# Kernel tuning notes

Measured on AMD Instinct MI355X. Metric: run time of the kernel, lower is better.

## Reference

```python
import jax, jax.numpy as jnp
import numpy as np

B, T, SLATE, D = 256, 16, 20, 256
N_ITEMS, N_USERS = 100000, 10000


def setup_inputs() -> dict:
    key = jax.random.key(0)
    ks = jax.random.split(key, 8)
    s = 1.0 / np.sqrt(D)  # PyTorch GRU/Linear init scale ~ U(-1/sqrt(H), 1/sqrt(H))
    return {
        "item_idxs": jax.random.randint(ks[0], (B, T, SLATE), 0, N_ITEMS),
        "user_idxs": jax.random.randint(ks[1], (B, T), 0, N_USERS),
        "responses": jnp.zeros((B, T, SLATE), jnp.float32),
        "item_table": jax.random.normal(ks[2], (N_ITEMS, D), jnp.float32) * 0.02,
        "user_table": jax.random.normal(ks[3], (N_USERS, D), jnp.float32) * 0.02,
        "W_ih": jax.random.uniform(ks[4], (3 * D, 2 * D), jnp.float32, -s, s),
        "W_hh": jax.random.uniform(ks[5], (3 * D, D), jnp.float32, -s, s),
        "b_ih": jnp.zeros((3 * D,), jnp.float32),
        "b_hh": jnp.zeros((3 * D,), jnp.float32),
        "W_out": jax.random.uniform(ks[6], (1, D), jnp.float32, -s, s),
        "b_out": jnp.zeros((1,), jnp.float32),
    }


def _gru_cell(x, h, W_ih, W_hh, b_ih, b_hh):
    # PyTorch GRUCell math. x: [N, 2D], h: [N, D]
    gi = x @ W_ih.T + b_ih  # [N, 3D]
    gh = h @ W_hh.T + b_hh  # [N, 3D]
    i_r, i_z, i_n = jnp.split(gi, 3, axis=-1)
    h_r, h_z, h_n = jnp.split(gh, 3, axis=-1)
    r = jax.nn.sigmoid(i_r + h_r)
    z = jax.nn.sigmoid(i_z + h_z)
    n = jnp.tanh(i_n + r * h_n)
    return (1.0 - z) * n + z * h


def reference(item_idxs, user_idxs, responses, item_table, user_table,
              W_ih, W_hh, b_ih, b_hh, W_out, b_out):
    # embedding lookup: item_embs [B,T,S,D], user_embs [B,T,D]
    item_embs = item_table[item_idxs]
    user_embs = user_table[user_idxs]
    N = B * T
    e = item_embs.reshape(N, SLATE, D).transpose(1, 0, 2)  # [S, N, D]
    h0 = user_embs.reshape(N, D)
    m0 = jnp.ones((N, 1), item_embs.dtype)  # 'soft' readout multiplier, 1 at step 0

    def step(carry, e_i):
        h, m = carry
        x = jnp.concatenate([e_i, e_i * m], axis=-1)  # [N, 2D]
        h = _gru_cell(x, h, W_ih, W_hh, b_ih, b_hh)
        y = h @ W_out.T + b_out  # [N, 1]
        return (h, jax.nn.sigmoid(y)), y[:, 0]

    _, ys = jax.lax.scan(step, (h0, m0), e)  # ys: [S, N]
    return ys.transpose(1, 0).reshape(B, T, SLATE)
```

## Files before the change

### kernel.cpp

```cpp
#include <hip/hip_runtime.h>
#include <math.h>

#define SLATE 20
#define DD 256
#define NSEQ 4096

typedef __attribute__((ext_vector_type(8))) short bf16x8;
typedef __attribute__((ext_vector_type(4))) float f32x4;
typedef unsigned short u16;
typedef unsigned int u32;

__device__ __forceinline__ u16 f2bf(float f) {
    unsigned u = __float_as_uint(f);
    u += 0x7fff + ((u >> 16) & 1);
    return (u16)(u >> 16);
}
__device__ __forceinline__ float blo(u32 u) { return __uint_as_float(u << 16); }
__device__ __forceinline__ float bhi(u32 u) { return __uint_as_float(u & 0xffff0000u); }
__device__ __forceinline__ float sigm_(float x) {
    return __builtin_amdgcn_rcpf(1.f + __builtin_amdgcn_exp2f(-1.44269504f * x));
}
__device__ __forceinline__ float tanh_(float x) {
    return 1.f - 2.f * __builtin_amdgcn_rcpf(1.f + __builtin_amdgcn_exp2f(2.88539008f * x));
}

__device__ __forceinline__ void gl_lds16(const void* g, void* l) {
    __builtin_amdgcn_global_load_lds(
        (const __attribute__((address_space(1))) unsigned int*)g,
        (__attribute__((address_space(3))) unsigned int*)l, 16, 0, 0);
}

__global__ void prep_w(const float* __restrict__ W_ih, const float* __restrict__ W_hh,
                       u16* __restrict__ W12, u16* __restrict__ Whh) {
    int i = blockIdx.x * 256 + threadIdx.x;
    if (i < 1536 * 256) {
        int j = i >> 8, k = i & 255;
        float v = (j < 768) ? W_ih[(size_t)j * 512 + k]
                            : W_ih[(size_t)(j - 768) * 512 + 256 + k];
        W12[i] = f2bf(v);
    } else {
        int i2 = i - 1536 * 256;
        Whh[i2] = f2bf(W_hh[i2]);
    }
}

__global__ void gather_e(int s0, const int* __restrict__ idxs, const float* __restrict__ itab,
                         u16* __restrict__ e_bf) {
    int g = blockIdx.x * 256 + threadIdx.x;
    int row = g >> 6, c = g & 63;
    int n = row & (NSEQ - 1), s = s0 + (row >> 12);
    int idx = idxs[n * SLATE + s];
    float4 v = *(const float4*)&itab[(size_t)idx * DD + c * 4];
    ushort4 o;
    o.x = f2bf(v.x); o.y = f2bf(v.y); o.z = f2bf(v.z); o.w = f2bf(v.w);
    *(ushort4*)&e_bf[(size_t)row * DD + c * 4] = o;
}

__global__ __launch_bounds__(256) void gemm_e(
        const u16* __restrict__ e_bf, const u16* __restrict__ W12,
        const float* __restrict__ b_ih, const float* __restrict__ b_hh,
        u16* __restrict__ Ge) {
    __shared__ u16 A_s[128][32];
    __shared__ u16 B_s[128][32];

    const int tid = threadIdx.x;
    const int w = tid >> 6, l = tid & 63, lm = l & 15, lq = l >> 4;
    const int wm = w & 1, wn = w >> 1;
    const size_t m0 = (size_t)blockIdx.y * 128;
    const size_t n0 = (size_t)blockIdx.x * 128;

    f32x4 acc[4][4];
    f32x4 zero4 = {0.f, 0.f, 0.f, 0.f};
#pragma unroll
    for (int mi = 0; mi < 4; ++mi)
#pragma unroll
        for (int nj = 0; nj < 4; ++nj) acc[mi][nj] = zero4;

    const int srow = w * 16 + (l >> 2);
    const int skc = (l & 3) * 8;
    const u16* gA = e_bf + (m0 + srow) * DD + skc;
    const u16* gB = W12 + (n0 + srow) * DD + skc;
    u16* lA = &A_s[0][0] + w * 512 + l * 8;
    u16* lB = &B_s[0][0] + w * 512 + l * 8;

    for (int kt = 0; kt < 8; ++kt) {
        const int ko = kt * 32;
        gl_lds16(gA + ko, lA);
        gl_lds16(gA + 64 * DD + ko, lA + 2048);
        gl_lds16(gB + ko, lB);
        gl_lds16(gB + 64 * DD + ko, lB + 2048);
        __syncthreads();
        bf16x8 af[4], bfr[4];
#pragma unroll
        for (int mi = 0; mi < 4; ++mi)
            af[mi] = *(const bf16x8*)&A_s[wm * 64 + mi * 16 + lm][lq * 8];
#pragma unroll
        for (int nj = 0; nj < 4; ++nj)
            bfr[nj] = *(const bf16x8*)&B_s[wn * 64 + nj * 16 + lm][lq * 8];
#pragma unroll
        for (int nj = 0; nj < 4; ++nj)
#pragma unroll
            for (int mi = 0; mi < 4; ++mi)
                acc[mi][nj] = __builtin_amdgcn_mfma_f32_16x16x32_bf16(af[mi], bfr[nj], acc[mi][nj], 0, 0, 0);
        __syncthreads();
    }
    float bb[4];
#pragma unroll
    for (int nj = 0; nj < 4; ++nj) {
        int col = (int)n0 + wn * 64 + nj * 16 + lm;
        bb[nj] = 0.f;
        if (col < 768) bb[nj] = b_ih[col] + (col < 512 ? b_hh[col] : 0.f);
    }
#pragma unroll
    for (int mi = 0; mi < 4; ++mi)
#pragma unroll
        for (int rr = 0; rr < 4; ++rr) {
            u16* gp = Ge + (m0 + wm * 64 + mi * 16 + lq * 4 + rr) * 1536 + n0 + wn * 64 + lm;
#pragma unroll
            for (int nj = 0; nj < 4; ++nj) gp[nj * 16] = f2bf(acc[mi][nj][rr] + bb[nj]);
        }
}

__device__ __forceinline__ int hA_off(int seq, int kt, int lq2) {
    int v = ((kt & 3) << 2) | lq2;
    return kt * 512 + lq2 * 128 + ((seq ^ v) << 3);
}

__global__ __launch_bounds__(512, 2) void seq_kernel(
        int s0, int C,
        const u16* __restrict__ Ge,
        const u16* __restrict__ Whh,
        const int* __restrict__ user_idxs, const float* __restrict__ user_table,
        const float* __restrict__ b_hh,
        const float* __restrict__ W_out, const float* __restrict__ b_out,
        float* __restrict__ h_g, float* __restrict__ m_g, float* __restrict__ out)
{
    __shared__ u16   hA[4096];
    __shared__ float gh_s[16][770];
    __shared__ u16   geL[2][16][1536];

    const int tid = threadIdx.x;
    const int w = tid >> 6, l = tid & 63, lm = l & 15, lq = l >> 4;
    const int l5 = l & 31, sh = l >> 5;
    const int n0 = blockIdx.x * 16;
    const int sloc = 2 * w + sh;
    const int nw = n0 + sloc;
    const int jw2 = w * 96;

    bf16x8 warr[6][8];
    const u16* wb = Whh + (size_t)(jw2 + lm) * DD + lq * 8;
#pragma unroll
    for (int fi = 0; fi < 6; ++fi)
#pragma unroll
        for (int kt = 0; kt < 8; ++kt)
            warr[fi][kt] = *(const bf16x8*)(wb + fi * 16 * DD + kt * 32);

    float bn[6];
#pragma unroll
    for (int fi = 0; fi < 6; ++fi) {
        int colb = jw2 + fi * 16;
        bn[fi] = (colb >= 512) ? b_hh[colb + lm] : 0.f;
    }

    float wo[8];
#pragma unroll
    for (int j = 0; j < 4; ++j) {
        float2 t = *(const float2*)&W_out[2 * l5 + 64 * j];
        wo[2 * j] = t.x; wo[2 * j + 1] = t.y;
    }
    const float bo = b_out[0];

    float h_reg[8]; float m_w;
    if (s0 == 0) {
        const float* hu = user_table + (size_t)user_idxs[nw] * DD;
#pragma unroll
        for (int j = 0; j < 4; ++j) {
            float2 t = *(const float2*)&hu[2 * l5 + 64 * j];
            h_reg[2 * j] = t.x; h_reg[2 * j + 1] = t.y;
        }
        m_w = 1.f;
    } else {
        const float* hp = h_g + (size_t)nw * DD;
#pragma unroll
        for (int j = 0; j < 4; ++j) {
            float2 t = *(const float2*)&hp[2 * l5 + 64 * j];
            h_reg[2 * j] = t.x; h_reg[2 * j + 1] = t.y;
        }
        m_w = m_g[nw];
    }
#pragma unroll
    for (int j = 0; j < 4; ++j) {
        int ktw = (l5 >> 4) + 2 * j, lq2 = (l5 & 15) >> 2;
        u32 pk = (u32)f2bf(h_reg[2 * j]) | ((u32)f2bf(h_reg[2 * j + 1]) << 16);
        *(u32*)&hA[hA_off(sloc, ktw, lq2) + 2 * (l5 & 3)] = pk;
    }

    {
        const u16* g0 = Ge + (size_t)n0 * 1536;
        u16* l0 = &geL[0][0][0];
#pragma unroll
        for (int i = 0; i < 6; ++i)
            gl_lds16(g0 + tid * 8 + i * 4096, l0 + tid * 8 + i * 4096);
    }
    asm volatile("s_waitcnt lgkmcnt(0)" ::: "memory");
    __builtin_amdgcn_s_barrier();
    __builtin_amdgcn_sched_barrier(0);

    for (int sc = 0; sc < C; ++sc) {
        const int cur = sc & 1;

        if (sc + 1 < C) {
            const u16* gn = Ge + ((size_t)(sc + 1) * NSEQ + n0) * 1536;
            u16* ln = &geL[cur ^ 1][0][0];
#pragma unroll
            for (int i = 0; i < 6; ++i)
                gl_lds16(gn + tid * 8 + i * 4096, ln + tid * 8 + i * 4096);
        }
        __builtin_amdgcn_sched_barrier(0);

        f32x4 zero4 = {0.f, 0.f, 0.f, 0.f};
        f32x4 acc[6];
#pragma unroll
        for (int fi = 0; fi < 6; ++fi) acc[fi] = zero4;
#pragma unroll
        for (int kt = 0; kt < 8; ++kt) {
            bf16x8 af = *(const bf16x8*)&hA[hA_off(lm, kt, lq)];
#pragma unroll
            for (int fi = 0; fi < 6; ++fi)
                acc[fi] = __builtin_amdgcn_mfma_f32_16x16x32_bf16(af, warr[fi][kt], acc[fi], 0, 0, 0);
        }
#pragma unroll
        for (int fi = 0; fi < 6; ++fi)
#pragma unroll
            for (int rr = 0; rr < 4; ++rr)
                gh_s[lq * 4 + rr][jw2 + fi * 16 + lm] = acc[fi][rr] + bn[fi];

        if (sc + 1 < C) { asm volatile("s_waitcnt vmcnt(6) lgkmcnt(0)" ::: "memory"); }
        else            { asm volatile("s_waitcnt vmcnt(0) lgkmcnt(0)" ::: "memory"); }
        __builtin_amdgcn_s_barrier();
        __builtin_amdgcn_sched_barrier(0);

        const u32* grow = (const u32*)&geL[cur][sloc][0];
        float yv = 0.f;
#pragma unroll
        for (int j = 0; j < 4; ++j) {
            u32 g1r = grow[      l5 + 32 * j];
            u32 g1z = grow[128 + l5 + 32 * j];
            u32 g1n = grow[256 + l5 + 32 * j];
            u32 g2r = grow[384 + l5 + 32 * j];
            u32 g2z = grow[512 + l5 + 32 * j];
            u32 g2n = grow[640 + l5 + 32 * j];
            const int d0 = 2 * l5 + 64 * j;
            float2 ghr = *(const float2*)&gh_s[sloc][d0];
            float2 ghz = *(const float2*)&gh_s[sloc][256 + d0];
            float2 ghn = *(const float2*)&gh_s[sloc][512 + d0];
            float ir_lo = fmaf(m_w, blo(g2r), blo(g1r));
            float ir_hi = fmaf(m_w, bhi(g2r), bhi(g1r));
            float iz_lo = fmaf(m_w, blo(g2z), blo(g1z));
            float iz_hi = fmaf(m_w, bhi(g2z), bhi(g1z));
            float in_lo = fmaf(m_w, blo(g2n), blo(g1n));
            float in_hi = fmaf(m_w, bhi(g2n), bhi(g1n));
            float r_lo = sigm_(ir_lo + ghr.x);
            float r_hi = sigm_(ir_hi + ghr.y);
            float z_lo = sigm_(iz_lo + ghz.x);
            float z_hi = sigm_(iz_hi + ghz.y);
            float n_lo = tanh_(fmaf(r_lo, ghn.x, in_lo));
            float n_hi = tanh_(fmaf(r_hi, ghn.y, in_hi));
            float hn_lo = fmaf(z_lo, h_reg[2 * j] - n_lo, n_lo);
            float hn_hi = fmaf(z_hi, h_reg[2 * j + 1] - n_hi, n_hi);
            h_reg[2 * j] = hn_lo; h_reg[2 * j + 1] = hn_hi;
            int ktw = (l5 >> 4) + 2 * j, lq2 = (l5 & 15) >> 2;
            u32 pk = (u32)f2bf(hn_lo) | ((u32)f2bf(hn_hi) << 16);
            *(u32*)&hA[hA_off(sloc, ktw, lq2) + 2 * (l5 & 3)] = pk;
            yv += hn_lo * wo[2 * j] + hn_hi * wo[2 * j + 1];
        }
#pragma unroll
        for (int off = 16; off > 0; off >>= 1) yv += __shfl_xor(yv, off, 32);
        float y = yv + bo;
        if (l5 == 0) out[(size_t)nw * SLATE + (s0 + sc)] = y;
        m_w = sigm_(y);

        asm volatile("s_waitcnt lgkmcnt(0)" ::: "memory");
        __builtin_amdgcn_s_barrier();
        __builtin_amdgcn_sched_barrier(0);
    }

#pragma unroll
    for (int j = 0; j < 4; ++j) {
        float2 v; v.x = h_reg[2 * j]; v.y = h_reg[2 * j + 1];
        *(float2*)&h_g[(size_t)nw * DD + 2 * l5 + 64 * j] = v;
    }
    if (l5 == 0) m_g[nw] = m_w;
}

extern "C" void kernel_launch(void* const* d_in, const int* in_sizes, int n_in,
                              void* d_out, int out_size, void* d_ws, size_t ws_size,
                              hipStream_t stream) {
    const int*   item_idxs  = (const int*)d_in[0];
    const int*   user_idxs  = (const int*)d_in[1];
    const float* item_table = (const float*)d_in[3];
    const float* user_table = (const float*)d_in[4];
    const float* W_ih       = (const float*)d_in[5];
    const float* W_hh       = (const float*)d_in[6];
    const float* b_ih       = (const float*)d_in[7];
    const float* b_hh       = (const float*)d_in[8];
    const float* W_out      = (const float*)d_in[9];
    const float* b_out      = (const float*)d_in[10];
    float* out = (float*)d_out;

    const size_t fixed = 786432ull + 393216ull + 4194304ull + 16384ull;
    static const int cands[5] = {10, 5, 4, 2, 1};
    int C = 1;
    for (int i = 0; i < 5; ++i) {
        size_t need = (size_t)cands[i] * (12582912ull + 2097152ull) + fixed;
        if (need <= ws_size) { C = cands[i]; break; }
    }

    u16*   Ge   = (u16*)d_ws;
    u16*   e_bf = (u16*)((char*)d_ws + (size_t)C * 12582912ull);
    u16*   W12  = (u16*)((char*)e_bf + (size_t)C * 2097152ull);
    u16*   Whh  = (u16*)((char*)W12 + 786432ull);
    float* h_g  = (float*)((char*)Whh + 393216ull);
    float* m_g  = (float*)((char*)h_g + 4194304ull);

    prep_w<<<2304, 256, 0, stream>>>(W_ih, W_hh, W12, Whh);

    for (int s0 = 0; s0 < SLATE; s0 += C) {
        gather_e<<<C * 1024, 256, 0, stream>>>(s0, item_idxs, item_table, e_bf);
        dim3 gg(12, 32 * C);
        gemm_e<<<gg, 256, 0, stream>>>(e_bf, W12, b_ih, b_hh, Ge);
        seq_kernel<<<256, 512, 0, stream>>>(s0, C, Ge, Whh, user_idxs, user_table,
                                            b_hh, W_out, b_out, h_g, m_g, out);
    }
}
```

Baseline: 399.2 us.

## Triple-buffer gemm_e LDS loads and vectorize transposed epilogue stores

The input-projection GEMM moves from a single-buffered LDS tile with two barriers per k-step to a three-stage ring. Loads run two k-steps ahead and are tracked with explicit vmcnt waits and one barrier per step. The MFMA operands are swapped so each lane holds four consecutive output columns, which lets the epilogue write packed 8-byte stores instead of scalar 2-byte stores, with the bias loaded before the loop. The cost is triple the LDS footprint and hand-written waitcnt logic that must match the async load count.

```diff
diff --git a/kernel.cpp b/kernel.cpp
--- a/kernel.cpp
+++ b/kernel.cpp
@@ -60,8 +60,8 @@
         const u16* __restrict__ e_bf, const u16* __restrict__ W12,
         const float* __restrict__ b_ih, const float* __restrict__ b_hh,
         u16* __restrict__ Ge) {
-    __shared__ u16 A_s[128][32];
-    __shared__ u16 B_s[128][32];
+    __shared__ u16 A_s[3][128][32];
+    __shared__ u16 B_s[3][128][32];
 
     const int tid = threadIdx.x;
     const int w = tid >> 6, l = tid & 63, lm = l & 15, lq = l >> 4;
@@ -69,6 +69,17 @@
     const size_t m0 = (size_t)blockIdx.y * 128;
     const size_t n0 = (size_t)blockIdx.x * 128;
 
+    float bb[4][4];
+#pragma unroll
+    for (int nj = 0; nj < 4; ++nj)
+#pragma unroll
+        for (int rr = 0; rr < 4; ++rr) {
+            int col = (int)n0 + wn * 64 + nj * 16 + lq * 4 + rr;
+            bb[nj][rr] = 0.f;
+            if (col < 768) bb[nj][rr] = b_ih[col] + (col < 512 ? b_hh[col] : 0.f);
+        }
+    __builtin_amdgcn_sched_barrier(0);
+
     f32x4 acc[4][4];
     f32x4 zero4 = {0.f, 0.f, 0.f, 0.f};
 #pragma unroll
@@ -80,45 +91,58 @@
     const int skc = (l & 3) * 8;
     const u16* gA = e_bf + (m0 + srow) * DD + skc;
     const u16* gB = W12 + (n0 + srow) * DD + skc;
-    u16* lA = &A_s[0][0] + w * 512 + l * 8;
-    u16* lB = &B_s[0][0] + w * 512 + l * 8;
-
+    const int loff = w * 512 + l * 8;
+
+#define STAGE_KT(bi, kk) do { const int ko_ = (kk) * 32;                     \
+        gl_lds16(gA + ko_,            &A_s[bi][0][0] + loff);                \
+        gl_lds16(gA + 64 * DD + ko_,  &A_s[bi][0][0] + loff + 2048);         \
+        gl_lds16(gB + ko_,            &B_s[bi][0][0] + loff);                \
+        gl_lds16(gB + 64 * DD + ko_,  &B_s[bi][0][0] + loff + 2048); } while (0)
+
+    STAGE_KT(0, 0);
+    STAGE_KT(1, 1);
+    asm volatile("s_waitcnt vmcnt(4)" ::: "memory");
+    __builtin_amdgcn_s_barrier();
+    __builtin_amdgcn_sched_barrier(0);
+
+#pragma unroll
     for (int kt = 0; kt < 8; ++kt) {
-        const int ko = kt * 32;
-        gl_lds16(gA + ko, lA);
-        gl_lds16(gA + 64 * DD + ko, lA + 2048);
-        gl_lds16(gB + ko, lB);
-        gl_lds16(gB + 64 * DD + ko, lB + 2048);
-        __syncthreads();
+        const int cur = kt % 3;
+        if (kt + 2 < 8) STAGE_KT((kt + 2) % 3, kt + 2);
+        __builtin_amdgcn_sched_barrier(0);
+
         bf16x8 af[4], bfr[4];
 #pragma unroll
         for (int mi = 0; mi < 4; ++mi)
-            af[mi] = *(const bf16x8*)&A_s[wm * 64 + mi * 16 + lm][lq * 8];
+            af[mi] = *(const bf16x8*)&A_s[cur][wm * 64 + mi * 16 + lm][lq * 8];
 #pragma unroll
         for (int nj = 0; nj < 4; ++nj)
-            bfr[nj] = *(const bf16x8*)&B_s[wn * 64 + nj * 16 + lm][lq * 8];
+            bfr[nj] = *(const bf16x8*)&B_s[cur][wn * 64 + nj * 16 + lm][lq * 8];
 #pragma unroll
         for (int nj = 0; nj < 4; ++nj)
 #pragma unroll
             for (int mi = 0; mi < 4; ++mi)
-                acc[mi][nj] = __builtin_amdgcn_mfma_f32_16x16x32_bf16(af[mi], bfr[nj], acc[mi][nj], 0, 0, 0);
-        __syncthreads();
-    }
-    float bb[4];
-#pragma unroll
-    for (int nj = 0; nj < 4; ++nj) {
-        int col = (int)n0 + wn * 64 + nj * 16 + lm;
-        bb[nj] = 0.f;
-        if (col < 768) bb[nj] = b_ih[col] + (col < 512 ? b_hh[col] : 0.f);
-    }
-#pragma unroll
-    for (int mi = 0; mi < 4; ++mi)
-#pragma unroll
-        for (int rr = 0; rr < 4; ++rr) {
-            u16* gp = Ge + (m0 + wm * 64 + mi * 16 + lq * 4 + rr) * 1536 + n0 + wn * 64 + lm;
-#pragma unroll
-            for (int nj = 0; nj < 4; ++nj) gp[nj * 16] = f2bf(acc[mi][nj][rr] + bb[nj]);
-        }
+                acc[mi][nj] = __builtin_amdgcn_mfma_f32_16x16x32_bf16(bfr[nj], af[mi], acc[mi][nj], 0, 0, 0);
+
+        if (kt < 6) { asm volatile("s_waitcnt vmcnt(4) lgkmcnt(0)" ::: "memory"); }
+        else        { asm volatile("s_waitcnt vmcnt(0) lgkmcnt(0)" ::: "memory"); }
+        __builtin_amdgcn_s_barrier();
+        __builtin_amdgcn_sched_barrier(0);
+    }
+#undef STAGE_KT
+
+#pragma unroll
+    for (int mi = 0; mi < 4; ++mi) {
+        const size_t row = m0 + wm * 64 + mi * 16 + lm;
+#pragma unroll
+        for (int nj = 0; nj < 4; ++nj) {
+            f32x4 a = acc[mi][nj];
+            u32 p0 = (u32)f2bf(a[0] + bb[nj][0]) | ((u32)f2bf(a[1] + bb[nj][1]) << 16);
+            u32 p1 = (u32)f2bf(a[2] + bb[nj][2]) | ((u32)f2bf(a[3] + bb[nj][3]) << 16);
+            uint2 v; v.x = p0; v.y = p1;
+            *(uint2*)(Ge + row * 1536 + n0 + wn * 64 + nj * 16 + lq * 4) = v;
+        }
+    }
 }
 
 __device__ __forceinline__ int hA_off(int seq, int kt, int lq2) {
```

Result: slower. 433.2 us (+8.5%).

## Enlarge gemm_e M-tile to 256 and vectorize transposed-output stores

Applied to the files above, without the earlier changes.

The input-projection GEMM now computes 256x128 tiles per block instead of 128x128, so each B tile loaded into LDS is reused across twice as many rows and the grid height is halved. The MFMA operands are swapped so each lane holds four consecutive output columns, which lets the epilogue pack bf16 pairs and write 8-byte stores instead of scattered 2-byte stores. Bias values are precomputed per lane before the K loop. Doubling the accumulators to 128 floats per thread raises register pressure, and the halved grid may lower occupancy. The sequential kernel is likely to dominate the total time anyway.

```diff
diff --git a/kernel.cpp b/kernel.cpp
--- a/kernel.cpp
+++ b/kernel.cpp
@@ -56,69 +56,77 @@
     *(ushort4*)&e_bf[(size_t)row * DD + c * 4] = o;
 }
 
-__global__ __launch_bounds__(256) void gemm_e(
+__global__ __launch_bounds__(256, 2) void gemm_e(
         const u16* __restrict__ e_bf, const u16* __restrict__ W12,
         const float* __restrict__ b_ih, const float* __restrict__ b_hh,
         u16* __restrict__ Ge) {
-    __shared__ u16 A_s[128][32];
+    __shared__ u16 A_s[256][32];
     __shared__ u16 B_s[128][32];
 
     const int tid = threadIdx.x;
     const int w = tid >> 6, l = tid & 63, lm = l & 15, lq = l >> 4;
     const int wm = w & 1, wn = w >> 1;
-    const size_t m0 = (size_t)blockIdx.y * 128;
+    const size_t m0 = (size_t)blockIdx.y * 256;
     const size_t n0 = (size_t)blockIdx.x * 128;
 
-    f32x4 acc[4][4];
+    float bb[4][4];
+#pragma unroll
+    for (int nj = 0; nj < 4; ++nj)
+#pragma unroll
+        for (int rr = 0; rr < 4; ++rr) {
+            int col = (int)n0 + wn * 64 + nj * 16 + lq * 4 + rr;
+            bb[nj][rr] = 0.f;
+            if (col < 768) bb[nj][rr] = b_ih[col] + (col < 512 ? b_hh[col] : 0.f);
+        }
+
+    f32x4 acc[8][4];
     f32x4 zero4 = {0.f, 0.f, 0.f, 0.f};
 #pragma unroll
-    for (int mi = 0; mi < 4; ++mi)
+    for (int mi = 0; mi < 8; ++mi)
 #pragma unroll
         for (int nj = 0; nj < 4; ++nj) acc[mi][nj] = zero4;
 
-    const int srow = w * 16 + (l >> 2);
-    const int skc = (l & 3) * 8;
-    const u16* gA = e_bf + (m0 + srow) * DD + skc;
-    const u16* gB = W12 + (n0 + srow) * DD + skc;
-    u16* lA = &A_s[0][0] + w * 512 + l * 8;
+    const u16* gA = e_bf + (m0 + (tid >> 2)) * DD + (tid & 3) * 8;
+    const u16* gB = W12 + (n0 + w * 16 + (l >> 2)) * DD + (l & 3) * 8;
+    u16* lA = &A_s[0][0] + tid * 8;
     u16* lB = &B_s[0][0] + w * 512 + l * 8;
 
     for (int kt = 0; kt < 8; ++kt) {
         const int ko = kt * 32;
-        gl_lds16(gA + ko, lA);
-        gl_lds16(gA + 64 * DD + ko, lA + 2048);
-        gl_lds16(gB + ko, lB);
-        gl_lds16(gB + 64 * DD + ko, lB + 2048);
+        gl_lds16(gA + ko,            lA);
+        gl_lds16(gA + 64 * DD + ko,  lA + 2048);
+        gl_lds16(gA + 128 * DD + ko, lA + 4096);
+        gl_lds16(gA + 192 * DD + ko, lA + 6144);
+        gl_lds16(gB + ko,            lB);
+        gl_lds16(gB + 64 * DD + ko,  lB + 2048);
         __syncthreads();
-        bf16x8 af[4], bfr[4];
-#pragma unroll
-        for (int mi = 0; mi < 4; ++mi)
-            af[mi] = *(const bf16x8*)&A_s[wm * 64 + mi * 16 + lm][lq * 8];
+        bf16x8 af[8], bfr[4];
+#pragma unroll
+        for (int mi = 0; mi < 8; ++mi)
+            af[mi] = *(const bf16x8*)&A_s[wm * 128 + mi * 16 + lm][lq * 8];
 #pragma unroll
         for (int nj = 0; nj < 4; ++nj)
             bfr[nj] = *(const bf16x8*)&B_s[wn * 64 + nj * 16 + lm][lq * 8];
 #pragma unroll
         for (int nj = 0; nj < 4; ++nj)
 #pragma unroll
-            for (int mi = 0; mi < 4; ++mi)
-                acc[mi][nj] = __builtin_amdgcn_mfma_f32_16x16x32_bf16(af[mi], bfr[nj], acc[mi][nj], 0, 0, 0);
+            for (int mi = 0; mi < 8; ++mi)
+                acc[mi][nj] = __builtin_amdgcn_mfma_f32_16x16x32_bf16(bfr[nj], af[mi], acc[mi][nj], 0, 0, 0);
         __syncthreads();
     }
-    float bb[4];
-#pragma unroll
-    for (int nj = 0; nj < 4; ++nj) {
-        int col = (int)n0 + wn * 64 + nj * 16 + lm;
-        bb[nj] = 0.f;
-        if (col < 768) bb[nj] = b_ih[col] + (col < 512 ? b_hh[col] : 0.f);
-    }
-#pragma unroll
-    for (int mi = 0; mi < 4; ++mi)
-#pragma unroll
-        for (int rr = 0; rr < 4; ++rr) {
-            u16* gp = Ge + (m0 + wm * 64 + mi * 16 + lq * 4 + rr) * 1536 + n0 + wn * 64 + lm;
-#pragma unroll
-            for (int nj = 0; nj < 4; ++nj) gp[nj * 16] = f2bf(acc[mi][nj][rr] + bb[nj]);
-        }
+
+#pragma unroll
+    for (int mi = 0; mi < 8; ++mi) {
+        const size_t row = m0 + wm * 128 + mi * 16 + lm;
+#pragma unroll
+        for (int nj = 0; nj < 4; ++nj) {
+            f32x4 a = acc[mi][nj];
+            u32 p0 = (u32)f2bf(a[0] + bb[nj][0]) | ((u32)f2bf(a[1] + bb[nj][1]) << 16);
+            u32 p1 = (u32)f2bf(a[2] + bb[nj][2]) | ((u32)f2bf(a[3] + bb[nj][3]) << 16);
+            uint2 v; v.x = p0; v.y = p1;
+            *(uint2*)(Ge + row * 1536 + n0 + wn * 64 + nj * 16 + lq * 4) = v;
+        }
+    }
 }
 
 __device__ __forceinline__ int hA_off(int seq, int kt, int lq2) {
@@ -327,7 +335,7 @@
 
     for (int s0 = 0; s0 < SLATE; s0 += C) {
         gather_e<<<C * 1024, 256, 0, stream>>>(s0, item_idxs, item_table, e_bf);
-        dim3 gg(12, 32 * C);
+        dim3 gg(12, 16 * C);
         gemm_e<<<gg, 256, 0, stream>>>(e_bf, W12, b_ih, b_hh, Ge);
         seq_kernel<<<256, 512, 0, stream>>>(s0, C, Ge, Whh, user_idxs, user_table,
                                             b_hh, W_out, b_out, h_g, m_g, out);
```

Measured after the change: 430.0 us. +7.7%, slower.

## Process 8 sequences per block in seq_kernel and double grid size

Applied to the files above, without the earlier changes.

The sequential GRU kernel now handles 8 sequences per block instead of 16, with one wave per sequence instead of half a wave, and launches 512 blocks instead of 256. The MFMA tile still covers 16 rows, so the upper 8 rows of the h operand are zeroed and half of the recurrent matmul work is wasted. The aim is to spread the serial recurrence over more CUs so that more of the mi355x's compute units stay busy, at the cost of doubling the per-sequence W_hh register loads and running MFMAs on padding rows.

```diff
diff --git a/kernel.cpp b/kernel.cpp
--- a/kernel.cpp
+++ b/kernel.cpp
@@ -136,15 +136,13 @@
         float* __restrict__ h_g, float* __restrict__ m_g, float* __restrict__ out)
 {
     __shared__ u16   hA[4096];
-    __shared__ float gh_s[16][770];
-    __shared__ u16   geL[2][16][1536];
+    __shared__ float gh_s[8][768];
+    __shared__ u16   geL[2][8][1536];
 
     const int tid = threadIdx.x;
     const int w = tid >> 6, l = tid & 63, lm = l & 15, lq = l >> 4;
-    const int l5 = l & 31, sh = l >> 5;
-    const int n0 = blockIdx.x * 16;
-    const int sloc = 2 * w + sh;
-    const int nw = n0 + sloc;
+    const int n0 = blockIdx.x * 8;
+    const int nw = n0 + w;
     const int jw2 = w * 96;
 
     bf16x8 warr[6][8];
@@ -162,44 +160,45 @@
         bn[fi] = (colb >= 512) ? b_hh[colb + lm] : 0.f;
     }
 
-    float wo[8];
-#pragma unroll
-    for (int j = 0; j < 4; ++j) {
-        float2 t = *(const float2*)&W_out[2 * l5 + 64 * j];
+    float wo[4];
+#pragma unroll
+    for (int j = 0; j < 2; ++j) {
+        float2 t = *(const float2*)&W_out[2 * l + 128 * j];
         wo[2 * j] = t.x; wo[2 * j + 1] = t.y;
     }
     const float bo = b_out[0];
 
-    float h_reg[8]; float m_w;
+    float h_reg[4]; float m_w;
     if (s0 == 0) {
         const float* hu = user_table + (size_t)user_idxs[nw] * DD;
 #pragma unroll
-        for (int j = 0; j < 4; ++j) {
-            float2 t = *(const float2*)&hu[2 * l5 + 64 * j];
+        for (int j = 0; j < 2; ++j) {
+            float2 t = *(const float2*)&hu[2 * l + 128 * j];
             h_reg[2 * j] = t.x; h_reg[2 * j + 1] = t.y;
         }
         m_w = 1.f;
     } else {
         const float* hp = h_g + (size_t)nw * DD;
 #pragma unroll
-        for (int j = 0; j < 4; ++j) {
-            float2 t = *(const float2*)&hp[2 * l5 + 64 * j];
+        for (int j = 0; j < 2; ++j) {
+            float2 t = *(const float2*)&hp[2 * l + 128 * j];
             h_reg[2 * j] = t.x; h_reg[2 * j + 1] = t.y;
         }
         m_w = m_g[nw];
     }
 #pragma unroll
-    for (int j = 0; j < 4; ++j) {
-        int ktw = (l5 >> 4) + 2 * j, lq2 = (l5 & 15) >> 2;
+    for (int j = 0; j < 2; ++j) {
+        int ktw = (l >> 4) + 4 * j, lq2 = (l >> 2) & 3;
         u32 pk = (u32)f2bf(h_reg[2 * j]) | ((u32)f2bf(h_reg[2 * j + 1]) << 16);
-        *(u32*)&hA[hA_off(sloc, ktw, lq2) + 2 * (l5 & 3)] = pk;
+        *(u32*)&hA[hA_off(w, ktw, lq2) + 2 * (l & 3)] = pk;
+        *(u32*)&hA[hA_off(w + 8, ktw, lq2) + 2 * (l & 3)] = 0u;
     }
 
     {
         const u16* g0 = Ge + (size_t)n0 * 1536;
         u16* l0 = &geL[0][0][0];
 #pragma unroll
-        for (int i = 0; i < 6; ++i)
+        for (int i = 0; i < 3; ++i)
             gl_lds16(g0 + tid * 8 + i * 4096, l0 + tid * 8 + i * 4096);
     }
     asm volatile("s_waitcnt lgkmcnt(0)" ::: "memory");
@@ -213,7 +212,7 @@
             const u16* gn = Ge + ((size_t)(sc + 1) * NSEQ + n0) * 1536;
             u16* ln = &geL[cur ^ 1][0][0];
 #pragma unroll
-            for (int i = 0; i < 6; ++i)
+            for (int i = 0; i < 3; ++i)
                 gl_lds16(gn + tid * 8 + i * 4096, ln + tid * 8 + i * 4096);
         }
         __builtin_amdgcn_sched_barrier(0);
@@ -229,31 +228,33 @@
             for (int fi = 0; fi < 6; ++fi)
                 acc[fi] = __builtin_amdgcn_mfma_f32_16x16x32_bf16(af, warr[fi][kt], acc[fi], 0, 0, 0);
         }
-#pragma unroll
-        for (int fi = 0; fi < 6; ++fi)
-#pragma unroll
-            for (int rr = 0; rr < 4; ++rr)
-                gh_s[lq * 4 + rr][jw2 + fi * 16 + lm] = acc[fi][rr] + bn[fi];
-
-        if (sc + 1 < C) { asm volatile("s_waitcnt vmcnt(6) lgkmcnt(0)" ::: "memory"); }
+        if (lq < 2) {
+#pragma unroll
+            for (int fi = 0; fi < 6; ++fi)
+#pragma unroll
+                for (int rr = 0; rr < 4; ++rr)
+                    gh_s[lq * 4 + rr][jw2 + fi * 16 + lm] = acc[fi][rr] + bn[fi];
+        }
+
+        if (sc + 1 < C) { asm volatile("s_waitcnt vmcnt(3) lgkmcnt(0)" ::: "memory"); }
         else            { asm volatile("s_waitcnt vmcnt(0) lgkmcnt(0)" ::: "memory"); }
         __builtin_amdgcn_s_barrier();
         __builtin_amdgcn_sched_barrier(0);
 
-        const u32* grow = (const u32*)&geL[cur][sloc][0];
+        const u32* grow = (const u32*)&geL[cur][w][0];
         float yv = 0.f;
 #pragma unroll
-        for (int j = 0; j < 4; ++j) {
-            u32 g1r = grow[      l5 + 32 * j];
-            u32 g1z = grow[128 + l5 + 32 * j];
-            u32 g1n = grow[256 + l5 + 32 * j];
-            u32 g2r = grow[384 + l5 + 32 * j];
-            u32 g2z = grow[512 + l5 + 32 * j];
-            u32 g2n = grow[640 + l5 + 32 * j];
-            const int d0 = 2 * l5 + 64 * j;
-            float2 ghr = *(const float2*)&gh_s[sloc][d0];
-            float2 ghz = *(const float2*)&gh_s[sloc][256 + d0];
-            float2 ghn = *(const float2*)&gh_s[sloc][512 + d0];
+        for (int j = 0; j < 2; ++j) {
+            u32 g1r = grow[      l + 64 * j];
+            u32 g1z = grow[128 + l + 64 * j];
+            u32 g1n = grow[256 + l + 64 * j];
+            u32 g2r = grow[384 + l + 64 * j];
+            u32 g2z = grow[512 + l + 64 * j];
+            u32 g2n = grow[640 + l + 64 * j];
+            const int d0 = 2 * l + 128 * j;
+            float2 ghr = *(const float2*)&gh_s[w][d0];
+            float2 ghz = *(const float2*)&gh_s[w][256 + d0];
+            float2 ghn = *(const float2*)&gh_s[w][512 + d0];
             float ir_lo = fmaf(m_w, blo(g2r), blo(g1r));
             float ir_hi = fmaf(m_w, bhi(g2r), bhi(g1r));
             float iz_lo = fmaf(m_w, blo(g2z), blo(g1z));
@@ -269,15 +270,15 @@
             float hn_lo = fmaf(z_lo, h_reg[2 * j] - n_lo, n_lo);
             float hn_hi = fmaf(z_hi, h_reg[2 * j + 1] - n_hi, n_hi);
             h_reg[2 * j] = hn_lo; h_reg[2 * j + 1] = hn_hi;
-            int ktw = (l5 >> 4) + 2 * j, lq2 = (l5 & 15) >> 2;
+            int ktw = (l >> 4) + 4 * j, lq2 = (l >> 2) & 3;
             u32 pk = (u32)f2bf(hn_lo) | ((u32)f2bf(hn_hi) << 16);
-            *(u32*)&hA[hA_off(sloc, ktw, lq2) + 2 * (l5 & 3)] = pk;
+            *(u32*)&hA[hA_off(w, ktw, lq2) + 2 * (l & 3)] = pk;
             yv += hn_lo * wo[2 * j] + hn_hi * wo[2 * j + 1];
         }
 #pragma unroll
-        for (int off = 16; off > 0; off >>= 1) yv += __shfl_xor(yv, off, 32);
+        for (int off = 32; off > 0; off >>= 1) yv += __shfl_xor(yv, off, 64);
         float y = yv + bo;
-        if (l5 == 0) out[(size_t)nw * SLATE + (s0 + sc)] = y;
+        if (l == 0) out[(size_t)nw * SLATE + (s0 + sc)] = y;
         m_w = sigm_(y);
 
         asm volatile("s_waitcnt lgkmcnt(0)" ::: "memory");
@@ -286,11 +287,11 @@
     }
 
 #pragma unroll
-    for (int j = 0; j < 4; ++j) {
+    for (int j = 0; j < 2; ++j) {
         float2 v; v.x = h_reg[2 * j]; v.y = h_reg[2 * j + 1];
-        *(float2*)&h_g[(size_t)nw * DD + 2 * l5 + 64 * j] = v;
-    }
-    if (l5 == 0) m_g[nw] = m_w;
+        *(float2*)&h_g[(size_t)nw * DD + 2 * l + 128 * j] = v;
+    }
+    if (l == 0) m_g[nw] = m_w;
 }
 
 extern "C" void kernel_launch(void* const* d_in, const int* in_sizes, int n_in,
@@ -329,7 +330,7 @@
         gather_e<<<C * 1024, 256, 0, stream>>>(s0, item_idxs, item_table, e_bf);
         dim3 gg(12, 32 * C);
         gemm_e<<<gg, 256, 0, stream>>>(e_bf, W12, b_ih, b_hh, Ge);
-        seq_kernel<<<256, 512, 0, stream>>>(s0, C, Ge, Whh, user_idxs, user_table,
+        seq_kernel<<<512, 512, 0, stream>>>(s0, C, Ge, Whh, user_idxs, user_table,
                                             b_hh, W_out, b_out, h_g, m_g, out);
     }
 }
```

Result: slower. 451.6 us (+13.1%).
